# Performance work log

Hardware: AMD Instinct MI355X
Metric: run time of the kernel (lower is better)

The kernel has to match this reference:

```python
import jax, jax.numpy as jnp
import numpy as np
import math

B, S, D, H = 2, 4096, 512, 8
DK = D // H


def setup_inputs() -> dict:
    key = jax.random.key(0)
    ks = jax.random.split(key, 9)
    s = 1.0 / math.sqrt(D)
    return {
        "x": jax.random.normal(ks[0], (B, S, D), dtype=jnp.float32),
        "Wq": jax.random.normal(ks[1], (D, D), dtype=jnp.float32) * s,
        "bq": jax.random.normal(ks[2], (D,), dtype=jnp.float32) * 0.01,
        "Wk": jax.random.normal(ks[3], (D, D), dtype=jnp.float32) * s,
        "bk": jax.random.normal(ks[4], (D,), dtype=jnp.float32) * 0.01,
        "Wv": jax.random.normal(ks[5], (D, D), dtype=jnp.float32) * s,
        "bv": jax.random.normal(ks[6], (D,), dtype=jnp.float32) * 0.01,
        "Wo": jax.random.normal(ks[7], (D, D), dtype=jnp.float32) * s,
        "bo": jax.random.normal(ks[8], (D,), dtype=jnp.float32) * 0.01,
    }


def reference(x, Wq, bq, Wk, bk, Wv, bv, Wo, bo):
    b, s, _ = x.shape
    # projections, split into heads: (b, h, s, dk)
    def proj(W, bias):
        return (x @ W.T + bias).reshape(b, s, H, DK).transpose(0, 2, 1, 3)
    Q, K, V = proj(Wq, bq), proj(Wk, bk), proj(Wv, bv)
    scale = 1.0 / math.sqrt(DK)
    scores = jnp.einsum("bhqd,bhkd->bhqk", Q, K) * scale  # (b,h,s,s)
    causal = jnp.tril(jnp.ones((s, s), dtype=bool))
    scores = jnp.where(causal[None, None], scores, -jnp.inf)
    attn = jax.nn.softmax(scores, axis=-1)
    out = jnp.einsum("bhqk,bhkd->bhqd", attn, V)
    out = out.transpose(0, 2, 1, 3).reshape(b, s, D)
    return out @ Wo.T + bo
```

## Files before the change

### kernel.cpp

```cpp
#include <hip/hip_runtime.h>
#include <hip/hip_bf16.h>

using u16    = unsigned short;
using u32    = unsigned int;
using bf16x8 = __attribute__((ext_vector_type(8))) __bf16;
using s16x4  = __attribute__((ext_vector_type(4))) short;
using f32x4  = __attribute__((ext_vector_type(4))) float;
using u16x4  = __attribute__((ext_vector_type(4))) unsigned short;
using u16x8  = __attribute__((ext_vector_type(8))) unsigned short;
using u32x2  = __attribute__((ext_vector_type(2))) unsigned int;
using u32x4  = __attribute__((ext_vector_type(4))) unsigned int;


static __device__ __forceinline__ u16 f2bf(float f) {
  unsigned int u = __float_as_uint(f);
  u += 0x7fffu + ((u >> 16) & 1u);
  return (u16)(u >> 16);
}
static __device__ __forceinline__ u32 pack2bf(float lo, float hi) {
  return __builtin_amdgcn_perm(__float_as_uint(hi), __float_as_uint(lo), 0x07060302u);
}

#if __has_builtin(__builtin_amdgcn_exp2f)
#define EXP2F(x) __builtin_amdgcn_exp2f(x)
#else
#define EXP2F(x) exp2f(x)
#endif

static __device__ __forceinline__ void gl_lds16(const u16* g, u16* l) {
  __builtin_amdgcn_global_load_lds(
      (const __attribute__((address_space(1))) unsigned int*)g,
      (__attribute__((address_space(3))) unsigned int*)l, 16, 0, 0);
}

__global__ __launch_bounds__(256) void cvt_all(
    const float* __restrict__ x,  const float* __restrict__ wq,
    const float* __restrict__ wk, const float* __restrict__ wv,
    const float* __restrict__ wo,
    u16* __restrict__ xb, u16* __restrict__ wqb, u16* __restrict__ wkb,
    u16* __restrict__ wvb, u16* __restrict__ wob) {
  const int bx = blockIdx.x;
  const float* src;
  u16* dst;
  int i;
  if (bx < 4096) {
    src = x; dst = xb; i = bx * 256 + threadIdx.x;
  } else {
    const int t  = (bx - 4096) >> 8;
    const int lb = (bx - 4096) & 255;
    src = (t == 0) ? wq : (t == 1) ? wk : (t == 2) ? wv : wo;
    dst = (t == 0) ? wqb : (t == 1) ? wkb : (t == 2) ? wvb : wob;
    i = lb * 256 + threadIdx.x;
  }
  float4 v = reinterpret_cast<const float4*>(src)[i];
  u16x4 o = { f2bf(v.x), f2bf(v.y), f2bf(v.z), f2bf(v.w) };
  reinterpret_cast<u16x4*>(dst)[i] = o;
}

__global__ __launch_bounds__(256, 3) void gemm_qkv(const u16* __restrict__ A,
                                                   const u16* __restrict__ Wq,
                                                   const u16* __restrict__ Wk,
                                                   const u16* __restrict__ Wv,
                                                   const float* __restrict__ bqp,
                                                   const float* __restrict__ bkp,
                                                   const float* __restrict__ bvp,
                                                   u16* __restrict__ Qo,
                                                   u16* __restrict__ Ko,
                                                   u16* __restrict__ Vto) {
  const int which = blockIdx.z;
  const u16* W = (which == 0) ? Wq : (which == 1) ? Wk : Wv;
  const float* bias = (which == 0) ? bqp : (which == 1) ? bkp : bvp;

  __shared__ u16 sA[128 * 72];
  __shared__ u16 sB[128 * 72];
  const int row0 = blockIdx.x * 128;
  const int col0 = blockIdx.y * 128;
  const int tid  = threadIdx.x;
  const int lane = tid & 63;
  const int wave = tid >> 6;
  const int wm   = (wave & 1) * 64;
  const int wn   = (wave >> 1) * 64;
  const int ln   = lane & 15;
  const int quad = lane >> 4;

  int rr[4], cc[4];
  for (int i = 0; i < 4; ++i) {
    const int idx = tid + 256 * i;
    rr[i] = idx >> 3; cc[i] = (idx & 7) * 8;
  }

  f32x4 zero = {0.f, 0.f, 0.f, 0.f};
  f32x4 acc[4][4];
  for (int i = 0; i < 4; ++i)
    for (int j = 0; j < 4; ++j) acc[i][j] = zero;

  u16x8 curA[4], nxtA[4], curB[4], nxtB[4];
  for (int i = 0; i < 4; ++i) {
    curA[i] = *reinterpret_cast<const u16x8*>(&A[(row0 + rr[i]) * 512 + cc[i]]);
    curB[i] = *reinterpret_cast<const u16x8*>(&W[(col0 + rr[i]) * 512 + cc[i]]);
  }

  for (int k0 = 0; k0 < 512; k0 += 64) {
    __syncthreads();
    for (int i = 0; i < 4; ++i) {
      *reinterpret_cast<u16x8*>(&sA[rr[i] * 72 + cc[i]]) = curA[i];
      *reinterpret_cast<u16x8*>(&sB[rr[i] * 72 + cc[i]]) = curB[i];
    }
    __syncthreads();
    if (k0 < 448)
      for (int i = 0; i < 4; ++i) {
        nxtA[i] = *reinterpret_cast<const u16x8*>(&A[(row0 + rr[i]) * 512 + k0 + 64 + cc[i]]);
        nxtB[i] = *reinterpret_cast<const u16x8*>(&W[(col0 + rr[i]) * 512 + k0 + 64 + cc[i]]);
      }
    for (int ks = 0; ks < 2; ++ks) {
      bf16x8 af[4], bfr[4];
      for (int t4 = 0; t4 < 4; ++t4)
        af[t4] = *reinterpret_cast<const bf16x8*>(&sA[(wm + t4 * 16 + ln) * 72 + ks * 32 + quad * 8]);
      for (int t4 = 0; t4 < 4; ++t4)
        bfr[t4] = *reinterpret_cast<const bf16x8*>(&sB[(wn + t4 * 16 + ln) * 72 + ks * 32 + quad * 8]);
      for (int tm = 0; tm < 4; ++tm)
        for (int tn = 0; tn < 4; ++tn)
          acc[tm][tn] = __builtin_amdgcn_mfma_f32_16x16x32_bf16(af[tm], bfr[tn], acc[tm][tn], 0, 0, 0);
    }
    for (int i = 0; i < 4; ++i) { curA[i] = nxtA[i]; curB[i] = nxtB[i]; }
  }

  if (which < 2) {
    u16* out = (which == 0) ? Qo : Ko;
    const float scale = (which == 0) ? 0.125f * 1.44269504088896f : 1.0f;
    for (int tm = 0; tm < 4; ++tm) {
      const int mbase = row0 + wm + tm * 16 + quad * 4;
      for (int tn = 0; tn < 4; ++tn) {
        const int n  = col0 + wn + tn * 16 + ln;
        const int h  = n >> 6, dk = n & 63;
        const float bv = bias[n];
        for (int r = 0; r < 4; ++r) {
          const int m  = mbase + r;
          const int bh = ((m >> 12) << 3) + h;
          const int s  = m & 4095;
          out[(bh * 4096 + s) * 64 + dk] = f2bf((acc[tm][tn][r] + bv) * scale);
        }
      }
    }
  } else {
    for (int tm = 0; tm < 4; ++tm) {
      const int mbase = row0 + wm + tm * 16 + quad * 4;
      const int b_idx = mbase >> 12;
      const int s     = mbase & 4095;
      for (int tn = 0; tn < 4; ++tn) {
        const int n  = col0 + wn + tn * 16 + ln;
        const int h  = n >> 6, dk = n & 63;
        const int bh = b_idx * 8 + h;
        const float bv = bias[n];
        u16x4 o;
        for (int r = 0; r < 4; ++r) o[r] = f2bf(acc[tm][tn][r] + bv);
        *reinterpret_cast<u16x4*>(&Vto[(bh * 64 + dk) * 4096 + s]) = o;
      }
    }
  }
}

__global__ __launch_bounds__(256, 3) void gemm_out(const u16* __restrict__ A,
                                                   const u16* __restrict__ W,
                                                   const float* __restrict__ bias,
                                                   float* __restrict__ out) {
  __shared__ u16 sA[128 * 72];
  __shared__ u16 sB[128 * 72];
  const int row0 = blockIdx.x * 128;
  const int col0 = blockIdx.y * 128;
  const int tid  = threadIdx.x;
  const int lane = tid & 63;
  const int wave = tid >> 6;
  const int wm   = (wave & 1) * 64;
  const int wn   = (wave >> 1) * 64;
  const int ln   = lane & 15;
  const int quad = lane >> 4;

  int rr[4], cc[4];
  for (int i = 0; i < 4; ++i) {
    const int idx = tid + 256 * i;
    rr[i] = idx >> 3; cc[i] = (idx & 7) * 8;
  }

  f32x4 zero = {0.f, 0.f, 0.f, 0.f};
  f32x4 acc[4][4];
  for (int i = 0; i < 4; ++i)
    for (int j = 0; j < 4; ++j) acc[i][j] = zero;

  u16x8 curA[4], nxtA[4], curB[4], nxtB[4];
  for (int i = 0; i < 4; ++i) {
    curA[i] = *reinterpret_cast<const u16x8*>(&A[(row0 + rr[i]) * 512 + cc[i]]);
    curB[i] = *reinterpret_cast<const u16x8*>(&W[(col0 + rr[i]) * 512 + cc[i]]);
  }

  for (int k0 = 0; k0 < 512; k0 += 64) {
    __syncthreads();
    for (int i = 0; i < 4; ++i) {
      *reinterpret_cast<u16x8*>(&sA[rr[i] * 72 + cc[i]]) = curA[i];
      *reinterpret_cast<u16x8*>(&sB[rr[i] * 72 + cc[i]]) = curB[i];
    }
    __syncthreads();
    if (k0 < 448)
      for (int i = 0; i < 4; ++i) {
        nxtA[i] = *reinterpret_cast<const u16x8*>(&A[(row0 + rr[i]) * 512 + k0 + 64 + cc[i]]);
        nxtB[i] = *reinterpret_cast<const u16x8*>(&W[(col0 + rr[i]) * 512 + k0 + 64 + cc[i]]);
      }
    for (int ks = 0; ks < 2; ++ks) {
      bf16x8 af[4], bfr[4];
      for (int t4 = 0; t4 < 4; ++t4)
        af[t4] = *reinterpret_cast<const bf16x8*>(&sA[(wm + t4 * 16 + ln) * 72 + ks * 32 + quad * 8]);
      for (int t4 = 0; t4 < 4; ++t4)
        bfr[t4] = *reinterpret_cast<const bf16x8*>(&sB[(wn + t4 * 16 + ln) * 72 + ks * 32 + quad * 8]);
      for (int tm = 0; tm < 4; ++tm)
        for (int tn = 0; tn < 4; ++tn)
          acc[tm][tn] = __builtin_amdgcn_mfma_f32_16x16x32_bf16(af[tm], bfr[tn], acc[tm][tn], 0, 0, 0);
    }
    for (int i = 0; i < 4; ++i) { curA[i] = nxtA[i]; curB[i] = nxtB[i]; }
  }

  for (int tm = 0; tm < 4; ++tm) {
    const int mbase = row0 + wm + tm * 16 + quad * 4;
    for (int tn = 0; tn < 4; ++tn) {
      const int n  = col0 + wn + tn * 16 + ln;
      const float bv = bias[n];
      for (int r = 0; r < 4; ++r)
        out[(mbase + r) * 512 + n] = acc[tm][tn][r] + bv;
    }
  }
}

#if __has_builtin(__builtin_amdgcn_mfma_f32_16x16x16bf16_1k)
#define HAVE_MFMA16 1
#endif
__global__ __launch_bounds__(256, 4) void attn_part(const u16* __restrict__ Q,
                                                    const u16* __restrict__ K,
                                                    const u16* __restrict__ Vt,
                                                    float* __restrict__ pO,
                                                    float* __restrict__ pl) {
  const int id = blockIdx.x;
  const int bh = id & 15;
  const int s  = 79 - (id >> 4);
  int t, c;
  if (s < 8)       { t = s;                 c = 0; }
  else if (s < 24) { const int u = s - 8;   t = 8  + (u >> 1); c = u & 1; }
  else if (s < 48) { const int u = s - 24;  const int q3 = u / 3; t = 16 + q3; c = u - 3 * q3; }
  else             { const int u = s - 48;  t = 24 + (u >> 2); c = u & 3; }

  const int nch = (t >> 3) + 1;
  const int ntiles = 2 * t + 2;
  const int len = (ntiles + nch - 1) / nch;
  const int kt0 = c * len;
  const int kt1e = kt0 + len;
  const int kt1 = ((kt1e < ntiles) ? kt1e : ntiles) - 1;
  const int qb = t * 128;

  const u16* Qh  = Q  + bh * 4096 * 64;
  const u16* Kh  = K  + bh * 4096 * 64;
  const u16* Vth = Vt + bh * 64 * 4096;

  __shared__ u16 sKb[2 * 64 * 64];
  __shared__ u16 sVb[2 * 64 * 64];

  const int tid  = threadIdx.x;
  const int lane = tid & 63;
  const int wave = tid >> 6;
  const int ln   = lane & 15;
  const int quad = lane >> 4;
  const int swz  = (lane & 7) << 3;

  const int e_src = 8 * ((lane & 7) ^ (lane >> 3));
  const int jr    = (wave << 4) + (lane >> 3);

  bf16x8 qf[2][2];
  for (int tn = 0; tn < 2; ++tn)
    for (int ks = 0; ks < 2; ++ks)
      qf[tn][ks] = *reinterpret_cast<const bf16x8*>(
          &Qh[(qb + wave * 32 + tn * 16 + ln) * 64 + ks * 32 + quad * 8]);

  f32x4 zero = {0.f, 0.f, 0.f, 0.f};
  f32x4 accO[4][2];
  float lsum[2] = {0.f, 0.f};
  for (int td = 0; td < 4; ++td)
    for (int tn = 0; tn < 2; ++tn) accO[td][tn] = zero;

#ifndef HAVE_MFMA16
  const int idx0 = 4 * (ln + 16 * (2 * (quad & 1)));
#endif

  auto stage = [&](int b, int kt) {
    u16* dK = &sKb[b * 4096];
    u16* dV = &sVb[b * 4096];
    const int kb = kt * 64;
    const int j0 = wave * 2;
    gl_lds16(&Kh[(kb + jr) * 64 + e_src],          &dK[j0 * 512]);
    gl_lds16(&Kh[(kb + jr + 8) * 64 + e_src],      &dK[(j0 + 1) * 512]);
    gl_lds16(&Vth[jr * 4096 + kb + e_src],         &dV[j0 * 512]);
    gl_lds16(&Vth[(jr + 8) * 4096 + kb + e_src],   &dV[(j0 + 1) * 512]);
  };

  stage(0, kt0);
  __syncthreads();

  int p = 0;
  for (int kt = kt0; kt <= kt1; ++kt, p ^= 1) {
    const int kb = kt * 64;
    if (kt < kt1) stage(p ^ 1, kt + 1);
    const u16* sK = &sKb[p * 4096];
    const u16* sV = &sVb[p * 4096];

    f32x4 accS[4][2];
    for (int tm = 0; tm < 4; ++tm)
      for (int tn = 0; tn < 2; ++tn) accS[tm][tn] = zero;
    __builtin_amdgcn_s_setprio(1);
    for (int tm = 0; tm < 4; ++tm) {
      bf16x8 kf0 = *reinterpret_cast<const bf16x8*>(&sK[(tm * 16 + ln) * 64 + ((quad * 8) ^ swz)]);
      bf16x8 kf1 = *reinterpret_cast<const bf16x8*>(&sK[(tm * 16 + ln) * 64 + ((32 + quad * 8) ^ swz)]);
      for (int tn = 0; tn < 2; ++tn) {
        accS[tm][tn] = __builtin_amdgcn_mfma_f32_16x16x32_bf16(kf0, qf[tn][0], accS[tm][tn], 0, 0, 0);
        accS[tm][tn] = __builtin_amdgcn_mfma_f32_16x16x32_bf16(kf1, qf[tn][1], accS[tm][tn], 0, 0, 0);
      }
    }
    __builtin_amdgcn_s_setprio(0);

    const bool diag = (kt >= 2 * t);
    u32 pp[4][2][2];
    for (int tm = 0; tm < 4; ++tm)
      for (int tn = 0; tn < 2; ++tn) {
        f32x4 e = accS[tm][tn];
        if (diag) {
          const int kg = kb + tm * 16 + quad * 4;
          const int qg = qb + wave * 32 + tn * 16 + ln;
          for (int r = 0; r < 4; ++r)
            if (kg + r > qg) e[r] = -__builtin_inff();
        }
        for (int r = 0; r < 4; ++r) e[r] = EXP2F(e[r]);
        lsum[tn] += (e[0] + e[1]) + (e[2] + e[3]);
        pp[tm][tn][0] = pack2bf(e[0], e[1]);
        pp[tm][tn][1] = pack2bf(e[2], e[3]);
      }

#ifdef HAVE_MFMA16
    __builtin_amdgcn_s_setprio(1);
    for (int k16 = 0; k16 < 4; ++k16)
      for (int td = 0; td < 4; ++td) {
        s16x4 vf = *reinterpret_cast<const s16x4*>(
            &sV[(td * 16 + ln) * 64 + ((k16 * 16 + quad * 4) ^ swz)]);
        for (int tn = 0; tn < 2; ++tn) {
          u32x2 pr = { pp[k16][tn][0], pp[k16][tn][1] };
          s16x4 pb = __builtin_bit_cast(s16x4, pr);
          accO[td][tn] = __builtin_amdgcn_mfma_f32_16x16x16bf16_1k(vf, pb, accO[td][tn], 0, 0, 0);
        }
      }
    __builtin_amdgcn_s_setprio(0);
#else
    for (int ks = 0; ks < 2; ++ks)
      for (int tn = 0; tn < 2; ++tn) {
        u32 b[4];
        for (int half = 0; half < 2; ++half)
          for (int pq = 0; pq < 2; ++pq) {
            int v0 = __builtin_amdgcn_ds_bpermute(idx0 + 64 * half, (int)pp[2 * ks][tn][pq]);
            int v1 = __builtin_amdgcn_ds_bpermute(idx0 + 64 * half, (int)pp[2 * ks + 1][tn][pq]);
            b[half * 2 + pq] = (quad < 2) ? (u32)v0 : (u32)v1;
          }
        u32x4 bv4 = { b[0], b[1], b[2], b[3] };
        bf16x8 pfrag = __builtin_bit_cast(bf16x8, bv4);
        __builtin_amdgcn_s_setprio(1);
        for (int td = 0; td < 4; ++td) {
          bf16x8 vf = *reinterpret_cast<const bf16x8*>(
              &sV[(td * 16 + ln) * 64 + ((ks * 32 + quad * 8) ^ swz)]);
          accO[td][tn] = __builtin_amdgcn_mfma_f32_16x16x32_bf16(vf, pfrag, accO[td][tn], 0, 0, 0);
        }
        __builtin_amdgcn_s_setprio(0);
      }
#endif

    if (kt < kt1) __syncthreads();
  }

  for (int tn = 0; tn < 2; ++tn) {
    lsum[tn] += __shfl_xor(lsum[tn], 16);
    lsum[tn] += __shfl_xor(lsum[tn], 32);
  }
  const int slot = bh * 80 + s;
  float* po = pO + (size_t)slot * 8192;
  for (int td = 0; td < 4; ++td)
    for (int tn = 0; tn < 2; ++tn)
      for (int r = 0; r < 4; ++r)
        po[(td * 16 + quad * 4 + r) * 128 + wave * 32 + tn * 16 + ln] = accO[td][tn][r];
  if (quad == 0)
    for (int tn = 0; tn < 2; ++tn)
      pl[slot * 128 + wave * 32 + tn * 16 + ln] = lsum[tn];
}

__global__ __launch_bounds__(256) void attn_comb(const float* __restrict__ pO,
                                                 const float* __restrict__ pl,
                                                 u16* __restrict__ ctx) {
  const int t  = blockIdx.x;
  const int bh = blockIdx.y;
  const int ga = t >> 3;
  const int nch = ga + 1;
  const int base = bh * 80 + t + 4 * ga * (ga - 1) + ga * (t & 7);
  const int tid = threadIdx.x;

  __shared__ float sO[64 * 132];
  __shared__ float sL[128];

  float4 acc[8];
  for (int i = 0; i < 8; ++i) acc[i] = make_float4(0.f, 0.f, 0.f, 0.f);
  float lacc = 0.f;
  for (int cidx = 0; cidx < nch; ++cidx) {
    const float* src = pO + (size_t)(base + cidx) * 8192;
    for (int i = 0; i < 8; ++i) {
      float4 v = reinterpret_cast<const float4*>(src)[i * 256 + tid];
      acc[i].x += v.x; acc[i].y += v.y; acc[i].z += v.z; acc[i].w += v.w;
    }
    if (tid < 128) lacc += pl[(base + cidx) * 128 + tid];
  }
  for (int i = 0; i < 8; ++i) {
    const int f = i * 256 + tid;
    const int d = f >> 5, q = (f & 31) * 4;
    *reinterpret_cast<float4*>(&sO[d * 132 + q]) = acc[i];
  }
  if (tid < 128) sL[tid] = lacc;
  __syncthreads();

  const int q  = tid >> 1;
  const int d0 = (tid & 1) * 32;
  const float inv = 1.0f / sL[q];
  const int b_idx = bh >> 3, h = bh & 7;
  const int tok = (b_idx << 12) + t * 128 + q;
  u16* dst = &ctx[tok * 512 + h * 64 + d0];
  for (int g = 0; g < 4; ++g) {
    u16x8 ov;
    for (int j = 0; j < 8; ++j) ov[j] = f2bf(sO[(d0 + g * 8 + j) * 132 + q] * inv);
    *reinterpret_cast<u16x8*>(&dst[g * 8]) = ov;
  }
}

extern "C" void kernel_launch(void* const* d_in, const int* in_sizes, int n_in,
                              void* d_out, int out_size, void* d_ws, size_t ws_size,
                              hipStream_t stream) {
  const float* x  = (const float*)d_in[0];
  const float* Wq = (const float*)d_in[1];
  const float* bq = (const float*)d_in[2];
  const float* Wk = (const float*)d_in[3];
  const float* bk = (const float*)d_in[4];
  const float* Wv = (const float*)d_in[5];
  const float* bv = (const float*)d_in[6];
  const float* Wo = (const float*)d_in[7];
  const float* bo = (const float*)d_in[8];
  float* out = (float*)d_out;

  char* ws = (char*)d_ws;
  u16* xb  = (u16*)(ws + 0);
  u16* wqb = (u16*)(ws + 8388608);
  u16* wkb = (u16*)(ws + 8912896);
  u16* wvb = (u16*)(ws + 9437184);
  u16* wob = (u16*)(ws + 9961472);
  u16* Qb  = (u16*)(ws + 10485760);
  u16* Kb  = (u16*)(ws + 18874368);
  u16* Vtb = (u16*)(ws + 27262976);
  float* pO = (float*)(ws + 35651584);
  float* pl = (float*)(ws + 77594624);
  u16* ctx = xb;

  cvt_all<<<5120, 256, 0, stream>>>(x, Wq, Wk, Wv, Wo, xb, wqb, wkb, wvb, wob);
  gemm_qkv<<<dim3(64, 4, 3), 256, 0, stream>>>(xb, wqb, wkb, wvb, bq, bk, bv, Qb, Kb, Vtb);
  attn_part<<<dim3(1280), 256, 0, stream>>>(Qb, Kb, Vtb, pO, pl);
  attn_comb<<<dim3(32, 16), 256, 0, stream>>>(pO, pl, ctx);
  gemm_out<<<dim3(64, 4), 256, 0, stream>>>(ctx, wob, bo, out);
}
```

Measured before the change: 186.6 us.

## Use direct global-to-LDS loads with XOR swizzle and staged epilogue in GEMMs

```diff
diff --git a/kernel.cpp b/kernel.cpp
--- a/kernel.cpp
+++ b/kernel.cpp
@@ -71,8 +71,10 @@
   const u16* W = (which == 0) ? Wq : (which == 1) ? Wk : Wv;
   const float* bias = (which == 0) ? bqp : (which == 1) ? bkp : bvp;
 
-  __shared__ u16 sA[128 * 72];
-  __shared__ u16 sB[128 * 72];
+  __shared__ u16 smem[2 * 128 * 64];
+  u16* sA = smem;
+  u16* sB = smem + 128 * 64;
+
   const int row0 = blockIdx.x * 128;
   const int col0 = blockIdx.y * 128;
   const int tid  = threadIdx.x;
@@ -82,81 +84,82 @@
   const int wn   = (wave >> 1) * 64;
   const int ln   = lane & 15;
   const int quad = lane >> 4;
-
-  int rr[4], cc[4];
-  for (int i = 0; i < 4; ++i) {
-    const int idx = tid + 256 * i;
-    rr[i] = idx >> 3; cc[i] = (idx & 7) * 8;
-  }
+  const int swz  = (ln & 7) << 3;
+
+  const int e_src = 8 * ((lane & 7) ^ (lane >> 3));
+  const int rloc  = lane >> 3;
 
   f32x4 zero = {0.f, 0.f, 0.f, 0.f};
   f32x4 acc[4][4];
   for (int i = 0; i < 4; ++i)
     for (int j = 0; j < 4; ++j) acc[i][j] = zero;
 
-  u16x8 curA[4], nxtA[4], curB[4], nxtB[4];
-  for (int i = 0; i < 4; ++i) {
-    curA[i] = *reinterpret_cast<const u16x8*>(&A[(row0 + rr[i]) * 512 + cc[i]]);
-    curB[i] = *reinterpret_cast<const u16x8*>(&W[(col0 + rr[i]) * 512 + cc[i]]);
-  }
-
   for (int k0 = 0; k0 < 512; k0 += 64) {
     __syncthreads();
-    for (int i = 0; i < 4; ++i) {
-      *reinterpret_cast<u16x8*>(&sA[rr[i] * 72 + cc[i]]) = curA[i];
-      *reinterpret_cast<u16x8*>(&sB[rr[i] * 72 + cc[i]]) = curB[i];
-    }
-    __syncthreads();
-    if (k0 < 448)
-      for (int i = 0; i < 4; ++i) {
-        nxtA[i] = *reinterpret_cast<const u16x8*>(&A[(row0 + rr[i]) * 512 + k0 + 64 + cc[i]]);
-        nxtB[i] = *reinterpret_cast<const u16x8*>(&W[(col0 + rr[i]) * 512 + k0 + 64 + cc[i]]);
-      }
+    for (int ch = 0; ch < 4; ++ch) {
+      const int j   = wave * 4 + ch;
+      const int row = j * 8 + rloc;
+      gl_lds16(&A[(row0 + row) * 512 + k0 + e_src], &sA[j * 512]);
+      gl_lds16(&W[(col0 + row) * 512 + k0 + e_src], &sB[j * 512]);
+    }
+    __syncthreads();
     for (int ks = 0; ks < 2; ++ks) {
       bf16x8 af[4], bfr[4];
       for (int t4 = 0; t4 < 4; ++t4)
-        af[t4] = *reinterpret_cast<const bf16x8*>(&sA[(wm + t4 * 16 + ln) * 72 + ks * 32 + quad * 8]);
+        af[t4] = *reinterpret_cast<const bf16x8*>(
+            &sA[(wm + t4 * 16 + ln) * 64 + ((ks * 32 + quad * 8) ^ swz)]);
       for (int t4 = 0; t4 < 4; ++t4)
-        bfr[t4] = *reinterpret_cast<const bf16x8*>(&sB[(wn + t4 * 16 + ln) * 72 + ks * 32 + quad * 8]);
+        bfr[t4] = *reinterpret_cast<const bf16x8*>(
+            &sB[(wn + t4 * 16 + ln) * 64 + ((ks * 32 + quad * 8) ^ swz)]);
       for (int tm = 0; tm < 4; ++tm)
         for (int tn = 0; tn < 4; ++tn)
           acc[tm][tn] = __builtin_amdgcn_mfma_f32_16x16x32_bf16(af[tm], bfr[tn], acc[tm][tn], 0, 0, 0);
     }
-    for (int i = 0; i < 4; ++i) { curA[i] = nxtA[i]; curB[i] = nxtB[i]; }
-  }
+  }
+
+  __syncthreads();
 
   if (which < 2) {
     u16* out = (which == 0) ? Qo : Ko;
     const float scale = (which == 0) ? 0.125f * 1.44269504088896f : 1.0f;
-    for (int tm = 0; tm < 4; ++tm) {
-      const int mbase = row0 + wm + tm * 16 + quad * 4;
+    for (int tm = 0; tm < 4; ++tm)
       for (int tn = 0; tn < 4; ++tn) {
-        const int n  = col0 + wn + tn * 16 + ln;
-        const int h  = n >> 6, dk = n & 63;
-        const float bv = bias[n];
+        const int nl = wn + tn * 16 + ln;
+        const float bv = bias[col0 + nl];
         for (int r = 0; r < 4; ++r) {
-          const int m  = mbase + r;
-          const int bh = ((m >> 12) << 3) + h;
-          const int s  = m & 4095;
-          out[(bh * 4096 + s) * 64 + dk] = f2bf((acc[tm][tn][r] + bv) * scale);
+          const int ml = wm + tm * 16 + quad * 4 + r;
+          smem[ml * 128 + (nl ^ ((ml & 7) << 3))] = f2bf((acc[tm][tn][r] + bv) * scale);
         }
       }
-    }
+    __syncthreads();
+    const int mrow = tid >> 1, half = tid & 1;
+    const int m  = row0 + mrow;
+    const int bh = ((m >> 12) << 3) + ((col0 + half * 64) >> 6);
+    u16* dst = &out[((size_t)bh * 4096 + (m & 4095)) * 64];
+    const int cswz = (mrow & 7) << 3;
+    for (int g = 0; g < 8; ++g)
+      *reinterpret_cast<u16x8*>(&dst[g * 8]) =
+          *reinterpret_cast<const u16x8*>(&smem[mrow * 128 + ((half * 64 + g * 8) ^ cswz)]);
   } else {
-    for (int tm = 0; tm < 4; ++tm) {
-      const int mbase = row0 + wm + tm * 16 + quad * 4;
-      const int b_idx = mbase >> 12;
-      const int s     = mbase & 4095;
+    for (int tm = 0; tm < 4; ++tm)
       for (int tn = 0; tn < 4; ++tn) {
-        const int n  = col0 + wn + tn * 16 + ln;
-        const int h  = n >> 6, dk = n & 63;
-        const int bh = b_idx * 8 + h;
-        const float bv = bias[n];
+        const int nl = wn + tn * 16 + ln;
+        const float bv = bias[col0 + nl];
+        const int mb = wm + tm * 16 + quad * 4;
         u16x4 o;
         for (int r = 0; r < 4; ++r) o[r] = f2bf(acc[tm][tn][r] + bv);
-        *reinterpret_cast<u16x4*>(&Vto[(bh * 64 + dk) * 4096 + s]) = o;
-      }
-    }
+        *reinterpret_cast<u16x4*>(&smem[nl * 128 + (mb ^ ((nl & 7) << 3))]) = o;
+      }
+    __syncthreads();
+    const int nrow = tid >> 1, mhalf = tid & 1;
+    const int n  = col0 + nrow;
+    const int bh = (row0 >> 12) * 8 + (n >> 6);
+    const int dk = n & 63;
+    u16* dst = &Vto[((size_t)(bh * 64 + dk)) * 4096 + (row0 & 4095) + mhalf * 64];
+    const int cswz = (nrow & 7) << 3;
+    for (int g = 0; g < 8; ++g)
+      *reinterpret_cast<u16x8*>(&dst[g * 8]) =
+          *reinterpret_cast<const u16x8*>(&smem[nrow * 128 + ((mhalf * 64 + g * 8) ^ cswz)]);
   }
 }
 
@@ -164,8 +167,10 @@
                                                    const u16* __restrict__ W,
                                                    const float* __restrict__ bias,
                                                    float* __restrict__ out) {
-  __shared__ u16 sA[128 * 72];
-  __shared__ u16 sB[128 * 72];
+  __shared__ u16 smem[2 * 128 * 64];
+  u16* sA = smem;
+  u16* sB = smem + 128 * 64;
+
   const int row0 = blockIdx.x * 128;
   const int col0 = blockIdx.y * 128;
   const int tid  = threadIdx.x;
@@ -175,47 +180,37 @@
   const int wn   = (wave >> 1) * 64;
   const int ln   = lane & 15;
   const int quad = lane >> 4;
-
-  int rr[4], cc[4];
-  for (int i = 0; i < 4; ++i) {
-    const int idx = tid + 256 * i;
-    rr[i] = idx >> 3; cc[i] = (idx & 7) * 8;
-  }
+  const int swz  = (ln & 7) << 3;
+
+  const int e_src = 8 * ((lane & 7) ^ (lane >> 3));
+  const int rloc  = lane >> 3;
 
   f32x4 zero = {0.f, 0.f, 0.f, 0.f};
   f32x4 acc[4][4];
   for (int i = 0; i < 4; ++i)
     for (int j = 0; j < 4; ++j) acc[i][j] = zero;
 
-  u16x8 curA[4], nxtA[4], curB[4], nxtB[4];
-  for (int i = 0; i < 4; ++i) {
-    curA[i] = *reinterpret_cast<const u16x8*>(&A[(row0 + rr[i]) * 512 + cc[i]]);
-    curB[i] = *reinterpret_cast<const u16x8*>(&W[(col0 + rr[i]) * 512 + cc[i]]);
-  }
-
   for (int k0 = 0; k0 < 512; k0 += 64) {
     __syncthreads();
-    for (int i = 0; i < 4; ++i) {
-      *reinterpret_cast<u16x8*>(&sA[rr[i] * 72 + cc[i]]) = curA[i];
-      *reinterpret_cast<u16x8*>(&sB[rr[i] * 72 + cc[i]]) = curB[i];
-    }
-    __syncthreads();
-    if (k0 < 448)
-      for (int i = 0; i < 4; ++i) {
-        nxtA[i] = *reinterpret_cast<const u16x8*>(&A[(row0 + rr[i]) * 512 + k0 + 64 + cc[i]]);
-        nxtB[i] = *reinterpret_cast<const u16x8*>(&W[(col0 + rr[i]) * 512 + k0 + 64 + cc[i]]);
-      }
+    for (int ch = 0; ch < 4; ++ch) {
+      const int j   = wave * 4 + ch;
+      const int row = j * 8 + rloc;
+      gl_lds16(&A[(row0 + row) * 512 + k0 + e_src], &sA[j * 512]);
+      gl_lds16(&W[(col0 + row) * 512 + k0 + e_src], &sB[j * 512]);
+    }
+    __syncthreads();
     for (int ks = 0; ks < 2; ++ks) {
       bf16x8 af[4], bfr[4];
       for (int t4 = 0; t4 < 4; ++t4)
-        af[t4] = *reinterpret_cast<const bf16x8*>(&sA[(wm + t4 * 16 + ln) * 72 + ks * 32 + quad * 8]);
+        af[t4] = *reinterpret_cast<const bf16x8*>(
+            &sA[(wm + t4 * 16 + ln) * 64 + ((ks * 32 + quad * 8) ^ swz)]);
       for (int t4 = 0; t4 < 4; ++t4)
-        bfr[t4] = *reinterpret_cast<const bf16x8*>(&sB[(wn + t4 * 16 + ln) * 72 + ks * 32 + quad * 8]);
+        bfr[t4] = *reinterpret_cast<const bf16x8*>(
+            &sB[(wn + t4 * 16 + ln) * 64 + ((ks * 32 + quad * 8) ^ swz)]);
       for (int tm = 0; tm < 4; ++tm)
         for (int tn = 0; tn < 4; ++tn)
           acc[tm][tn] = __builtin_amdgcn_mfma_f32_16x16x32_bf16(af[tm], bfr[tn], acc[tm][tn], 0, 0, 0);
     }
-    for (int i = 0; i < 4; ++i) { curA[i] = nxtA[i]; curB[i] = nxtB[i]; }
   }
 
   for (int tm = 0; tm < 4; ++tm) {
```

New measurement: 185.6 us. No clear change (-0.5%).

## Split attention into fixed 8-tile KV chunks, store partials in bf16, drop double buffering

Applied to the files above, without the earlier changes.

```diff
diff --git a/kernel.cpp b/kernel.cpp
--- a/kernel.cpp
+++ b/kernel.cpp
@@ -235,22 +235,20 @@
 __global__ __launch_bounds__(256, 4) void attn_part(const u16* __restrict__ Q,
                                                     const u16* __restrict__ K,
                                                     const u16* __restrict__ Vt,
-                                                    float* __restrict__ pO,
+                                                    u16* __restrict__ pO,
                                                     float* __restrict__ pl) {
   const int id = blockIdx.x;
   const int bh = id & 15;
-  const int s  = 79 - (id >> 4);
-  int t, c;
-  if (s < 8)       { t = s;                 c = 0; }
-  else if (s < 24) { const int u = s - 8;   t = 8  + (u >> 1); c = u & 1; }
-  else if (s < 48) { const int u = s - 24;  const int q3 = u / 3; t = 16 + q3; c = u - 3 * q3; }
-  else             { const int u = s - 48;  t = 24 + (u >> 2); c = u & 3; }
-
-  const int nch = (t >> 3) + 1;
+  const int s  = 143 - (id >> 4);
+  int g = 0;
+  while (s >= 2 * (g + 1) * (g + 2)) ++g;
+  const int u  = s - 2 * g * (g + 1);
+  const int t  = 4 * g + u / (g + 1);
+  const int c  = u % (g + 1);
+
   const int ntiles = 2 * t + 2;
-  const int len = (ntiles + nch - 1) / nch;
-  const int kt0 = c * len;
-  const int kt1e = kt0 + len;
+  const int kt0 = 8 * c;
+  const int kt1e = kt0 + 8;
   const int kt1 = ((kt1e < ntiles) ? kt1e : ntiles) - 1;
   const int qb = t * 128;
 
@@ -258,8 +256,8 @@
   const u16* Kh  = K  + bh * 4096 * 64;
   const u16* Vth = Vt + bh * 64 * 4096;
 
-  __shared__ u16 sKb[2 * 64 * 64];
-  __shared__ u16 sVb[2 * 64 * 64];
+  __shared__ u16 sK[64 * 64];
+  __shared__ u16 sV[64 * 64];
 
   const int tid  = threadIdx.x;
   const int lane = tid & 63;
@@ -287,26 +285,17 @@
   const int idx0 = 4 * (ln + 16 * (2 * (quad & 1)));
 #endif
 
-  auto stage = [&](int b, int kt) {
-    u16* dK = &sKb[b * 4096];
-    u16* dV = &sVb[b * 4096];
+  for (int kt = kt0; kt <= kt1; ++kt) {
     const int kb = kt * 64;
-    const int j0 = wave * 2;
-    gl_lds16(&Kh[(kb + jr) * 64 + e_src],          &dK[j0 * 512]);
-    gl_lds16(&Kh[(kb + jr + 8) * 64 + e_src],      &dK[(j0 + 1) * 512]);
-    gl_lds16(&Vth[jr * 4096 + kb + e_src],         &dV[j0 * 512]);
-    gl_lds16(&Vth[(jr + 8) * 4096 + kb + e_src],   &dV[(j0 + 1) * 512]);
-  };
-
-  stage(0, kt0);
-  __syncthreads();
-
-  int p = 0;
-  for (int kt = kt0; kt <= kt1; ++kt, p ^= 1) {
-    const int kb = kt * 64;
-    if (kt < kt1) stage(p ^ 1, kt + 1);
-    const u16* sK = &sKb[p * 4096];
-    const u16* sV = &sVb[p * 4096];
+    if (kt > kt0) __syncthreads();
+    {
+      const int j0 = wave * 2;
+      gl_lds16(&Kh[(kb + jr) * 64 + e_src],          &sK[j0 * 512]);
+      gl_lds16(&Kh[(kb + jr + 8) * 64 + e_src],      &sK[(j0 + 1) * 512]);
+      gl_lds16(&Vth[jr * 4096 + kb + e_src],         &sV[j0 * 512]);
+      gl_lds16(&Vth[(jr + 8) * 4096 + kb + e_src],   &sV[(j0 + 1) * 512]);
+    }
+    __syncthreads();
 
     f32x4 accS[4][2];
     for (int tm = 0; tm < 4; ++tm)
@@ -373,53 +362,56 @@
         __builtin_amdgcn_s_setprio(0);
       }
 #endif
-
-    if (kt < kt1) __syncthreads();
   }
 
   for (int tn = 0; tn < 2; ++tn) {
     lsum[tn] += __shfl_xor(lsum[tn], 16);
     lsum[tn] += __shfl_xor(lsum[tn], 32);
   }
-  const int slot = bh * 80 + s;
-  float* po = pO + (size_t)slot * 8192;
+  const int slot = bh * 144 + s;
+  u16* po = pO + (size_t)slot * 8192;
   for (int td = 0; td < 4; ++td)
     for (int tn = 0; tn < 2; ++tn)
       for (int r = 0; r < 4; ++r)
-        po[(td * 16 + quad * 4 + r) * 128 + wave * 32 + tn * 16 + ln] = accO[td][tn][r];
+        po[(td * 16 + quad * 4 + r) * 128 + wave * 32 + tn * 16 + ln] = f2bf(accO[td][tn][r]);
   if (quad == 0)
     for (int tn = 0; tn < 2; ++tn)
       pl[slot * 128 + wave * 32 + tn * 16 + ln] = lsum[tn];
 }
 
-__global__ __launch_bounds__(256) void attn_comb(const float* __restrict__ pO,
+__global__ __launch_bounds__(256) void attn_comb(const u16* __restrict__ pO,
                                                  const float* __restrict__ pl,
                                                  u16* __restrict__ ctx) {
   const int t  = blockIdx.x;
   const int bh = blockIdx.y;
-  const int ga = t >> 3;
-  const int nch = ga + 1;
-  const int base = bh * 80 + t + 4 * ga * (ga - 1) + ga * (t & 7);
+  const int g  = t >> 2;
+  const int nch = g + 1;
+  const int base = bh * 144 + 2 * g * (g + 1) + (t & 3) * (g + 1);
   const int tid = threadIdx.x;
 
   __shared__ float sO[64 * 132];
   __shared__ float sL[128];
 
-  float4 acc[8];
-  for (int i = 0; i < 8; ++i) acc[i] = make_float4(0.f, 0.f, 0.f, 0.f);
+  float accv[4][8];
+  for (int i = 0; i < 4; ++i)
+    for (int j = 0; j < 8; ++j) accv[i][j] = 0.f;
   float lacc = 0.f;
   for (int cidx = 0; cidx < nch; ++cidx) {
-    const float* src = pO + (size_t)(base + cidx) * 8192;
-    for (int i = 0; i < 8; ++i) {
-      float4 v = reinterpret_cast<const float4*>(src)[i * 256 + tid];
-      acc[i].x += v.x; acc[i].y += v.y; acc[i].z += v.z; acc[i].w += v.w;
+    const u16* src = pO + (size_t)(base + cidx) * 8192;
+    for (int i = 0; i < 4; ++i) {
+      u16x8 h = reinterpret_cast<const u16x8*>(src)[i * 256 + tid];
+      for (int j = 0; j < 8; ++j)
+        accv[i][j] += __uint_as_float(((u32)h[j]) << 16);
     }
     if (tid < 128) lacc += pl[(base + cidx) * 128 + tid];
   }
-  for (int i = 0; i < 8; ++i) {
-    const int f = i * 256 + tid;
-    const int d = f >> 5, q = (f & 31) * 4;
-    *reinterpret_cast<float4*>(&sO[d * 132 + q]) = acc[i];
+  for (int i = 0; i < 4; ++i) {
+    const int e0 = (i * 256 + tid) * 8;
+    const int d = e0 >> 7, q = e0 & 127;
+    float4 lo = make_float4(accv[i][0], accv[i][1], accv[i][2], accv[i][3]);
+    float4 hi = make_float4(accv[i][4], accv[i][5], accv[i][6], accv[i][7]);
+    *reinterpret_cast<float4*>(&sO[d * 132 + q])     = lo;
+    *reinterpret_cast<float4*>(&sO[d * 132 + q + 4]) = hi;
   }
   if (tid < 128) sL[tid] = lacc;
   __syncthreads();
@@ -430,10 +422,10 @@
   const int b_idx = bh >> 3, h = bh & 7;
   const int tok = (b_idx << 12) + t * 128 + q;
   u16* dst = &ctx[tok * 512 + h * 64 + d0];
-  for (int g = 0; g < 4; ++g) {
+  for (int gg = 0; gg < 4; ++gg) {
     u16x8 ov;
-    for (int j = 0; j < 8; ++j) ov[j] = f2bf(sO[(d0 + g * 8 + j) * 132 + q] * inv);
-    *reinterpret_cast<u16x8*>(&dst[g * 8]) = ov;
+    for (int j = 0; j < 8; ++j) ov[j] = f2bf(sO[(d0 + gg * 8 + j) * 132 + q] * inv);
+    *reinterpret_cast<u16x8*>(&dst[gg * 8]) = ov;
   }
 }
 
@@ -460,13 +452,13 @@
   u16* Qb  = (u16*)(ws + 10485760);
   u16* Kb  = (u16*)(ws + 18874368);
   u16* Vtb = (u16*)(ws + 27262976);
-  float* pO = (float*)(ws + 35651584);
-  float* pl = (float*)(ws + 77594624);
+  u16*   pO = (u16*)(ws + 35651584);
+  float* pl = (float*)(ws + 73400320);
   u16* ctx = xb;
 
   cvt_all<<<5120, 256, 0, stream>>>(x, Wq, Wk, Wv, Wo, xb, wqb, wkb, wvb, wob);
   gemm_qkv<<<dim3(64, 4, 3), 256, 0, stream>>>(xb, wqb, wkb, wvb, bq, bk, bv, Qb, Kb, Vtb);
-  attn_part<<<dim3(1280), 256, 0, stream>>>(Qb, Kb, Vtb, pO, pl);
+  attn_part<<<dim3(2304), 256, 0, stream>>>(Qb, Kb, Vtb, pO, pl);
   attn_comb<<<dim3(32, 16), 256, 0, stream>>>(pO, pl, ctx);
   gemm_out<<<dim3(64, 4), 256, 0, stream>>>(ctx, wob, bo, out);
 }
```

Result: faster. 173.6 us (-7.0%).
